# Performance work log

Hardware: AMD Instinct MI355X
Metric: run time of the kernel (lower is better)

## Reference

```python
import jax, jax.numpy as jnp
import numpy as np

HEADS = 8
HEAD_DIM = 64
INNER = HEADS * HEAD_DIM  # 512
DIM = 512
B, H, W = 8, 32, 32
KV_LEN, KV_DIM = 77, 1024


def group_norm(x, g, b, groups=32, eps=1e-6):
    # x: [B, C, H, W]
    Bx, C, Hx, Wx = x.shape
    xr = x.reshape(Bx, groups, C // groups, Hx, Wx)
    mu = xr.mean(axis=(2, 3, 4), keepdims=True)
    var = xr.var(axis=(2, 3, 4), keepdims=True)
    xr = (xr - mu) * jax.lax.rsqrt(var + eps)
    return xr.reshape(Bx, C, Hx, Wx) * g[None, :, None, None] + b[None, :, None, None]


def layer_norm(x, g, b, eps=1e-5):
    mu = x.mean(axis=-1, keepdims=True)
    var = x.var(axis=-1, keepdims=True)
    return (x - mu) * jax.lax.rsqrt(var + eps) * g + b


def attention(qx, kvx, Wq, Wk, Wv, Wo, bo):
    # qx: [B, Sq, dim_q], kvx: [B, Sk, dim_kv]
    q = qx @ Wq
    k = kvx @ Wk
    v = kvx @ Wv
    Bx, Sq, _ = q.shape
    Sk = k.shape[1]
    q = q.reshape(Bx, Sq, HEADS, HEAD_DIM)
    k = k.reshape(Bx, Sk, HEADS, HEAD_DIM)
    v = v.reshape(Bx, Sk, HEADS, HEAD_DIM)
    att = jnp.einsum('bqhd,bkhd->bhqk', q, k) * (HEAD_DIM ** -0.5)
    att = jax.nn.softmax(att.astype(jnp.float32), axis=-1).astype(q.dtype)
    o = jnp.einsum('bhqk,bkhd->bqhd', att, v).reshape(Bx, Sq, INNER)
    return o @ Wo + bo


def setup_inputs() -> dict:
    key = jax.random.key(0)
    ks = jax.random.split(key, 20)
    s = 0.02
    def n(k, shape):
        return jax.random.normal(k, shape, jnp.float32) * s
    return {
        'q': jax.random.normal(ks[0], (B, DIM, H, W), jnp.float32),
        'kv': jax.random.normal(ks[1], (B, KV_LEN, KV_DIM), jnp.float32),
        'gn_g': jnp.ones((DIM,), jnp.float32), 'gn_b': jnp.zeros((DIM,), jnp.float32),
        'ln2_g': jnp.ones((INNER,), jnp.float32), 'ln2_b': jnp.zeros((INNER,), jnp.float32),
        'ln3_g': jnp.ones((INNER,), jnp.float32), 'ln3_b': jnp.zeros((INNER,), jnp.float32),
        'ln4_g': jnp.ones((INNER,), jnp.float32), 'ln4_b': jnp.zeros((INNER,), jnp.float32),
        'fc_in_w': n(ks[2], (DIM, INNER)), 'fc_in_b': jnp.zeros((INNER,), jnp.float32),
        'fc_out_w': n(ks[3], (INNER, DIM)), 'fc_out_b': jnp.zeros((DIM,), jnp.float32),
        'a1_q': n(ks[4], (INNER, INNER)), 'a1_k': n(ks[5], (INNER, INNER)),
        'a1_v': n(ks[6], (INNER, INNER)), 'a1_o': n(ks[7], (INNER, INNER)),
        'a1_ob': jnp.zeros((INNER,), jnp.float32),
        'a2_q': n(ks[8], (INNER, INNER)), 'a2_k': n(ks[9], (KV_DIM, INNER)),
        'a2_v': n(ks[10], (KV_DIM, INNER)), 'a2_o': n(ks[11], (INNER, INNER)),
        'a2_ob': jnp.zeros((INNER,), jnp.float32),
        'ff_proj_w': n(ks[12], (INNER, INNER * 8)), 'ff_proj_b': jnp.zeros((INNER * 8,), jnp.float32),
        'ff_out_w': n(ks[13], (INNER * 4, INNER)), 'ff_out_b': jnp.zeros((INNER,), jnp.float32),
    }


def reference(q, kv, gn_g, gn_b, ln2_g, ln2_b, ln3_g, ln3_b, ln4_g, ln4_b,
              fc_in_w, fc_in_b, fc_out_w, fc_out_b,
              a1_q, a1_k, a1_v, a1_o, a1_ob,
              a2_q, a2_k, a2_v, a2_o, a2_ob,
              ff_proj_w, ff_proj_b, ff_out_w, ff_out_b):
    res = q
    Bx, C, Hx, Wx = q.shape
    x = group_norm(q, gn_g, gn_b)
    x = x.reshape(Bx, C, Hx * Wx).transpose(0, 2, 1)  # [B, S, C]
    x = x @ fc_in_w + fc_in_b
    t = layer_norm(x, ln2_g, ln2_b)
    x = attention(t, t, a1_q, a1_k, a1_v, a1_o, a1_ob) + x
    x = attention(layer_norm(x, ln3_g, ln3_b), kv, a2_q, a2_k, a2_v, a2_o, a2_ob) + x
    h = layer_norm(x, ln4_g, ln4_b) @ ff_proj_w + ff_proj_b
    a, gate = jnp.split(h, 2, axis=-1)
    x = (a * jax.nn.gelu(gate, approximate=False)) @ ff_out_w + ff_out_b + x
    x = x @ fc_out_w + fc_out_b
    x = x.transpose(0, 2, 1).reshape(Bx, C, Hx, Wx)
    return x + res
```

## Files before the change

### kernel.cpp

```cpp
#include <hip/hip_runtime.h>
#include <cstdint>
#include <cstddef>

typedef __attribute__((ext_vector_type(8))) short bf16x8;
typedef __attribute__((ext_vector_type(4))) short short4v;
typedef __attribute__((ext_vector_type(4))) float f32x4;

__device__ __forceinline__ short f2b(float f) {
    unsigned u = __builtin_bit_cast(unsigned, f);
    u = (u + 0x7FFFu + ((u >> 16) & 1u)) >> 16;
    return (short)u;
}
__device__ __forceinline__ float b2f(short s) {
    unsigned u = ((unsigned)(unsigned short)s) << 16;
    return __builtin_bit_cast(float, u);
}

__device__ __forceinline__ void gload16(const short* g, short* l) {
    __builtin_amdgcn_global_load_lds(
        (const __attribute__((address_space(1))) unsigned int*)g,
        (__attribute__((address_space(3))) unsigned int*)l, 16, 0, 0);
}

__device__ __forceinline__ float gelu_fast(float g) {
    float g2 = g * g;
    float gp = g * (0.7978845608f + 0.0356774081f * g2);
    float e = exp2f(2.885390082f * gp);
    float th = 1.f - 2.f / (e + 1.f);
    return 0.5f * g * (1.f + th);
}

__device__ __forceinline__ int pn_ffp(int n) {
    int m = (n < 2048) ? n : (n - 2048);
    int gofs = (n < 2048) ? 0 : 32;
    int x = m >> 6, c = m & 63;
    return x * 128 + ((c >> 5) << 6) + gofs + (c & 31);
}

struct PrepArgs {
    const float* src[12];
    short* dst[12];
    const float* kv;
    short* kvb;
    const float* fb;
    float* bp;
};

__global__ __launch_bounds__(256) void prep(PrepArgs a) {
    int t = blockIdx.x;
    int tid = threadIdx.x;
    if (t >= 6144) {
        if (t >= 6452) {
            int n = (t - 6452) * 256 + tid;
            if (n < 4096) a.bp[pn_ffp(n)] = a.fb[n];
            return;
        }
        int idx = (t - 6144) * 256 + tid;
        if (idx >= 78848) return;
        const float4* s = (const float4*)a.kv + (size_t)idx * 2;
        float4 va = s[0], vb = s[1];
        bf16x8 w;
        w[0] = f2b(va.x); w[1] = f2b(va.y); w[2] = f2b(va.z); w[3] = f2b(va.w);
        w[4] = f2b(vb.x); w[5] = f2b(vb.y); w[6] = f2b(vb.z); w[7] = f2b(vb.w);
        *(bf16x8*)(a.kvb + (size_t)idx * 8) = w;
        return;
    }
    const int jstart[12] = {0, 256, 512, 768, 1024, 1280, 1536, 1792, 2304, 2816, 3072, 5120};
    const int jK[12] = {512, 512, 512, 512, 512, 512, 512, 1024, 1024, 512, 512, 2048};
    const int jN[12] = {512, 512, 512, 512, 512, 512, 512, 512, 512, 512, 4096, 512};
    int j = 11;
#pragma unroll
    for (int i = 11; i >= 1; --i)
        if (t < jstart[i]) j = i - 1;
    int tx = t - jstart[j];
    int K = jK[j], N = jN[j];
    int tn = N >> 5;
    int n0 = (tx % tn) * 32, k0 = (tx / tn) * 32;
    const float* w = a.src[j];
    short* wt = a.dst[j];
    bool perm = (j == 10);

    __shared__ float tile[32][33];
    int cx = tid & 31, ty0 = tid >> 5;
#pragma unroll
    for (int i = 0; i < 4; ++i) {
        int r = ty0 + i * 8;
        tile[r][cx] = w[(size_t)(k0 + r) * N + n0 + cx];
    }
    __syncthreads();
    int r = tid >> 3;
    int kg = (tid & 7) * 4;
    int drow = perm ? pn_ffp(n0 + r) : (n0 + r);
    short4v o = {f2b(tile[kg][r]), f2b(tile[kg + 1][r]),
                 f2b(tile[kg + 2][r]), f2b(tile[kg + 3][r])};
    *(short4v*)&wt[(size_t)drow * K + k0 + kg] = o;
}

__global__ __launch_bounds__(256) void gn_stats(const float* __restrict__ q,
                                                const float* __restrict__ g,
                                                const float* __restrict__ bta,
                                                float* __restrict__ sc,
                                                float* __restrict__ sh) {
    int bb = blockIdx.x >> 5, gg = blockIdx.x & 31;
    const float4* src = (const float4*)(q + ((size_t)(bb * 512 + gg * 16)) * 1024);
    float s = 0.f, s2 = 0.f;
#pragma unroll
    for (int i = 0; i < 16; ++i) {
        float4 v = src[threadIdx.x + 256 * i];
        s += (v.x + v.y) + (v.z + v.w);
        s2 += (v.x * v.x + v.y * v.y) + (v.z * v.z + v.w * v.w);
    }
#pragma unroll
    for (int m = 1; m < 64; m <<= 1) {
        s += __shfl_xor(s, m);
        s2 += __shfl_xor(s2, m);
    }
    __shared__ float red[8];
    int wv = threadIdx.x >> 6;
    if ((threadIdx.x & 63) == 0) { red[wv] = s; red[4 + wv] = s2; }
    __syncthreads();
    if (threadIdx.x < 16) {
        float S = red[0] + red[1] + red[2] + red[3];
        float S2 = red[4] + red[5] + red[6] + red[7];
        float mu = S * (1.f / 16384.f);
        float var = S2 * (1.f / 16384.f) - mu * mu;
        float rs = rsqrtf(var + 1e-6f);
        int c = gg * 16 + threadIdx.x;
        float scale = rs * g[c];
        sc[bb * 512 + c] = scale;
        sh[bb * 512 + c] = bta[c] - mu * scale;
    }
}

__global__ __launch_bounds__(256) void gn_apply(const float* __restrict__ q,
                                                const float* __restrict__ sc,
                                                const float* __restrict__ sh,
                                                short* __restrict__ out) {
    __shared__ short tile[512][33];
    int b = blockIdx.x >> 5, st = blockIdx.x & 31;
    int s0 = st * 32;
    int sl = threadIdx.x & 31, cg = threadIdx.x >> 5;
    for (int c = cg; c < 512; c += 8) {
        float v = q[((size_t)(b * 512 + c)) * 1024 + s0 + sl];
        float y = v * sc[b * 512 + c] + sh[b * 512 + c];
        tile[c][sl] = f2b(y);
    }
    __syncthreads();
    int sr = threadIdx.x >> 3, ch = threadIdx.x & 7;
    short* orow = out + ((size_t)(b * 1024 + s0 + sr)) * 512;
    for (int c8 = ch * 64; c8 < ch * 64 + 64; c8 += 8) {
        bf16x8 o;
#pragma unroll
        for (int jj = 0; jj < 8; ++jj) o[jj] = tile[c8 + jj][sr];
        *(bf16x8*)&orow[c8] = o;
    }
}

__global__ __launch_bounds__(256) void ln_rows(const short* __restrict__ x,
                                               const float* __restrict__ g,
                                               const float* __restrict__ bta,
                                               short* __restrict__ out) {
    int row = blockIdx.x * 4 + (threadIdx.x >> 6);
    int lane = threadIdx.x & 63;
    bf16x8 v8 = *(const bf16x8*)(x + (size_t)row * 512 + lane * 8);
    float v[8];
#pragma unroll
    for (int j = 0; j < 8; ++j) v[j] = b2f(v8[j]);
    float s = 0.f, s2 = 0.f;
#pragma unroll
    for (int j = 0; j < 8; ++j) { s += v[j]; s2 += v[j] * v[j]; }
#pragma unroll
    for (int m = 1; m < 64; m <<= 1) {
        s += __shfl_xor(s, m);
        s2 += __shfl_xor(s2, m);
    }
    float mu = s * (1.f / 512.f);
    float var = s2 * (1.f / 512.f) - mu * mu;
    float rs = rsqrtf(var + 1e-5f);
    float4 ga = ((const float4*)g)[lane * 2], gb = ((const float4*)g)[lane * 2 + 1];
    float4 ba = ((const float4*)bta)[lane * 2], bb = ((const float4*)bta)[lane * 2 + 1];
    bf16x8 o;
    o[0] = f2b((v[0] - mu) * rs * ga.x + ba.x);
    o[1] = f2b((v[1] - mu) * rs * ga.y + ba.y);
    o[2] = f2b((v[2] - mu) * rs * ga.z + ba.z);
    o[3] = f2b((v[3] - mu) * rs * ga.w + ba.w);
    o[4] = f2b((v[4] - mu) * rs * gb.x + bb.x);
    o[5] = f2b((v[5] - mu) * rs * gb.y + bb.y);
    o[6] = f2b((v[6] - mu) * rs * gb.z + bb.z);
    o[7] = f2b((v[7] - mu) * rs * gb.w + bb.w);
    *(bf16x8*)(out + (size_t)row * 512 + lane * 8) = o;
}

template <int BN>
__global__ __launch_bounds__(256, 1) void gemm_gl(
    const short* __restrict__ A, const short* __restrict__ BT,
    int M, int N, int K,
    const float* __restrict__ bias,
    const short* __restrict__ addSrcB,
    short* __restrict__ outB,
    const float* __restrict__ resid,
    float* __restrict__ outFinal,
    int mode) {
    constexpr int FJ = BN / 32;
    constexpr int ASZ = 3 * 128 * 32;
    constexpr int BSZ = 3 * BN * 32;
    __shared__ __attribute__((aligned(16))) short smem[ASZ + BSZ];
    short* Asb = smem;
    short* Bsb = smem + ASZ;
    int tid = threadIdx.x;
    int wave = tid >> 6, lane = tid & 63;
    int wr = wave >> 1, wc = wave & 1;
    int m0 = blockIdx.y * 128, n0 = blockIdx.x * BN;
    f32x4 acc[4][FJ];
#pragma unroll
    for (int i = 0; i < 4; ++i)
#pragma unroll
        for (int j = 0; j < FJ; ++j) acc[i][j] = (f32x4){0.f, 0.f, 0.f, 0.f};

    int srow = tid >> 2;
    int scg = (((tid & 3) ^ ((tid >> 3) & 3)) << 3);
    int ar0 = m0 + srow; if (ar0 >= M) ar0 = M - 1;
    int ar1 = m0 + 64 + srow; if (ar1 >= M) ar1 = M - 1;
    const short* ag0 = A + (size_t)ar0 * K + scg;
    const short* ag1 = A + (size_t)ar1 * K + scg;
    const short* bg0 = BT + (size_t)(n0 + srow) * K + scg;
    const short* bg1 = BT + (size_t)(n0 + 64 + srow) * K + scg;
    int nk = K >> 5;

    auto stage = [&](int buf) {
        gload16(ag0, &Asb[buf * 4096 + wave * 512]);
        gload16(ag1, &Asb[buf * 4096 + 2048 + wave * 512]);
        gload16(bg0, &Bsb[buf * (BN * 32) + wave * 512]);
        if constexpr (BN == 128) gload16(bg1, &Bsb[buf * 4096 + 2048 + wave * 512]);
        ag0 += 32; ag1 += 32; bg0 += 32; bg1 += 32;
    };
    stage(0);
    stage(1);

    int lr = lane & 15, g = lane >> 4;

#define GL_STEP(KT, BUF)                                                          \
    {                                                                             \
        __builtin_amdgcn_sched_barrier(0);                                        \
        if ((KT) + 1 < nk) {                                                      \
            if constexpr (BN == 128)                                              \
                asm volatile("s_waitcnt vmcnt(4)" ::: "memory");                  \
            else                                                                  \
                asm volatile("s_waitcnt vmcnt(3)" ::: "memory");                  \
        } else {                                                                  \
            asm volatile("s_waitcnt vmcnt(0)" ::: "memory");                      \
        }                                                                         \
        __builtin_amdgcn_sched_barrier(0);                                        \
        __builtin_amdgcn_s_barrier();                                             \
        if ((KT) + 2 < nk) stage(((BUF) + 2) % 3);                                \
        bf16x8 af[4], bfr[FJ];                                                    \
        _Pragma("unroll") for (int i = 0; i < 4; ++i) {                           \
            int row = wr * 64 + i * 16 + lr;                                      \
            af[i] = *(const bf16x8*)&Asb[(BUF) * 4096 + row * 32 +                \
                                         ((g ^ ((row >> 1) & 3)) << 3)];          \
        }                                                                         \
        _Pragma("unroll") for (int j = 0; j < FJ; ++j) {                          \
            int row = wc * (BN / 2) + j * 16 + lr;                                \
            bfr[j] = *(const bf16x8*)&Bsb[(BUF) * (BN * 32) + row * 32 +          \
                                          ((g ^ ((row >> 1) & 3)) << 3)];         \
        }                                                                         \
        _Pragma("unroll") for (int i = 0; i < 4; ++i)                             \
            _Pragma("unroll") for (int j = 0; j < FJ; ++j)                        \
                acc[i][j] = __builtin_amdgcn_mfma_f32_16x16x32_bf16(              \
                    af[i], bfr[j], acc[i][j], 0, 0, 0);                           \
    }

    for (int kt = 0; kt < nk; kt += 3) {
        GL_STEP(kt, 0);
        if (kt + 1 < nk) GL_STEP(kt + 1, 1);
        if (kt + 2 < nk) GL_STEP(kt + 2, 2);
    }
#undef GL_STEP

    int lq = lane >> 4;
    if (mode == 1) {
#pragma unroll
        for (int i = 0; i < 4; ++i)
#pragma unroll
            for (int j = 0; j < FJ; ++j) {
                int mm0 = m0 + wr * 64 + i * 16 + lq * 4;
                int nn = n0 + wc * (BN / 2) + j * 16 + lr;
                int bb = mm0 >> 10, ss = mm0 & 1023;
                size_t oi = ((size_t)(bb * 512 + nn)) * 1024 + ss;
                float bv = bias ? bias[nn] : 0.f;
                float4 rv = *(const float4*)&resid[oi];
                float4 ov;
                ov.x = acc[i][j][0] + bv + rv.x;
                ov.y = acc[i][j][1] + bv + rv.y;
                ov.z = acc[i][j][2] + bv + rv.z;
                ov.w = acc[i][j][3] + bv + rv.w;
                *(float4*)&outFinal[oi] = ov;
            }
        return;
    }
    {
        constexpr int EC = BN + 4;
        float* ef = (float*)smem;
#pragma unroll
        for (int h = 0; h < 2; ++h) {
            __syncthreads();
            if (wr == h) {
#pragma unroll
                for (int i = 0; i < 4; ++i)
#pragma unroll
                    for (int j = 0; j < FJ; ++j)
#pragma unroll
                        for (int r = 0; r < 4; ++r)
                            ef[(i * 16 + lq * 4 + r) * EC + wc * (BN / 2) + j * 16 + lr] =
                                acc[i][j][r];
            }
            __syncthreads();
#pragma unroll
            for (int q = 0; q < BN / 16; ++q) {
                int idx = q * 256 + tid;
                int row = idx / (BN / 4);
                int cq = (idx % (BN / 4)) * 4;
                int mm = m0 + h * 64 + row;
                if (mm >= M) continue;
                int nn = n0 + cq;
                float4 v = *(float4*)&ef[row * EC + cq];
                if (bias) {
                    float4 b4 = *(const float4*)&bias[nn];
                    v.x += b4.x; v.y += b4.y; v.z += b4.z; v.w += b4.w;
                }
                size_t ig = (size_t)mm * N + nn;
                if (addSrcB) {
                    short4v a4 = *(const short4v*)&addSrcB[ig];
                    v.x += b2f(a4[0]); v.y += b2f(a4[1]);
                    v.z += b2f(a4[2]); v.w += b2f(a4[3]);
                }
                short4v o = {f2b(v.x), f2b(v.y), f2b(v.z), f2b(v.w)};
                *(short4v*)&outB[ig] = o;
            }
        }
    }
}

__global__ __launch_bounds__(512, 1) void gemm256w(
    const short* __restrict__ A, const short* __restrict__ BT,
    int M, int N, int K,
    const float* __restrict__ bias,
    short* __restrict__ outB,
    int mode) {
    __shared__ __attribute__((aligned(16))) short smem[3 * 4096 + 3 * 8192];
    short* Asb = smem;
    short* Bsb = smem + 12288;
    int tid = threadIdx.x;
    int wave = tid >> 6, lane = tid & 63;
    int wrM = wave >> 2, wcN = wave & 3;
    int m0 = blockIdx.y * 128, n0 = blockIdx.x * 256;
    f32x4 acc[4][4];
#pragma unroll
    for (int i = 0; i < 4; ++i)
#pragma unroll
        for (int j = 0; j < 4; ++j) acc[i][j] = (f32x4){0.f, 0.f, 0.f, 0.f};

    const short* gp[3];
    int ldsoff[3];
    bool isA[3];
#pragma unroll
    for (int s = 0; s < 3; ++s) {
        int qq = wave * 3 + s;
        bool a = qq < 8;
        int r = (a ? qq : qq - 8) * 16 + (lane >> 2);
        int sc = (((lane & 3) ^ ((r >> 1) & 3)) << 3);
        gp[s] = a ? (A + (size_t)(m0 + r) * K + sc)
                  : (BT + (size_t)(n0 + r) * K + sc);
        ldsoff[s] = (a ? qq : (qq - 8)) * 512;
        isA[s] = a;
    }
    int nk = K >> 5;
    auto stage = [&](int buf) {
#pragma unroll
        for (int s = 0; s < 3; ++s) {
            short* l = isA[s] ? &Asb[buf * 4096 + ldsoff[s]]
                              : &Bsb[buf * 8192 + ldsoff[s]];
            gload16(gp[s], l);
            gp[s] += 32;
        }
    };
    stage(0);
    stage(1);

    int lr = lane & 15, g = lane >> 4;

#define W8_STEP(KT, BUF)                                                          \
    {                                                                             \
        __builtin_amdgcn_sched_barrier(0);                                        \
        if ((KT) + 1 < nk) {                                                      \
            asm volatile("s_waitcnt vmcnt(3)" ::: "memory");                      \
        } else {                                                                  \
            asm volatile("s_waitcnt vmcnt(0)" ::: "memory");                      \
        }                                                                         \
        __builtin_amdgcn_sched_barrier(0);                                        \
        __builtin_amdgcn_s_barrier();                                             \
        if ((KT) + 2 < nk) stage(((BUF) + 2) % 3);                                \
        bf16x8 af[4], bfr[4];                                                     \
        _Pragma("unroll") for (int i = 0; i < 4; ++i) {                           \
            int row = wrM * 64 + i * 16 + lr;                                     \
            af[i] = *(const bf16x8*)&Asb[(BUF) * 4096 + row * 32 +                \
                                         ((g ^ ((row >> 1) & 3)) << 3)];          \
        }                                                                         \
        _Pragma("unroll") for (int j = 0; j < 4; ++j) {                           \
            int row = wcN * 64 + j * 16 + lr;                                     \
            bfr[j] = *(const bf16x8*)&Bsb[(BUF) * 8192 + row * 32 +               \
                                          ((g ^ ((row >> 1) & 3)) << 3)];         \
        }                                                                         \
        _Pragma("unroll") for (int i = 0; i < 4; ++i)                             \
            _Pragma("unroll") for (int j = 0; j < 4; ++j)                         \
                acc[i][j] = __builtin_amdgcn_mfma_f32_16x16x32_bf16(              \
                    af[i], bfr[j], acc[i][j], 0, 0, 0);                           \
    }

    for (int kt = 0; kt < nk; kt += 3) {
        W8_STEP(kt, 0);
        if (kt + 1 < nk) W8_STEP(kt + 1, 1);
        if (kt + 2 < nk) W8_STEP(kt + 2, 2);
    }
#undef W8_STEP

    int lq = lane >> 4;
    if (mode == 2) {
        short* eb = smem;
        int xhalf = wcN >> 1, half = wcN & 1;
        __syncthreads();
#pragma unroll
        for (int i = 0; i < 4; ++i)
#pragma unroll
            for (int j = 0; j < 2; ++j)
#pragma unroll
                for (int r = 0; r < 4; ++r) {
                    int slot = n0 + wcN * 64 + j * 16 + lr;
                    float a = acc[i][j][r] + bias[slot];
                    float gt = acc[i][j + 2][r] + bias[slot + 32];
                    float ge = gelu_fast(gt);
                    int row = wrM * 64 + i * 16 + lq * 4 + r;
                    int col = xhalf * 64 + half * 32 + j * 16 + lr;
                    eb[row * 136 + col] = f2b(a * ge);
                }
        __syncthreads();
#pragma unroll
        for (int q = 0; q < 4; ++q) {
            int idx = q * 512 + tid;
            int row = idx >> 4, cg = (idx & 15) * 8;
            bf16x8 o = *(bf16x8*)&eb[row * 136 + cg];
            *(bf16x8*)&outB[(size_t)(m0 + row) * 2048 + blockIdx.x * 128 + cg] = o;
        }
        return;
    }
    {
        float* ef = (float*)smem;
#pragma unroll
        for (int h = 0; h < 2; ++h) {
            __syncthreads();
            if (wrM == h) {
#pragma unroll
                for (int i = 0; i < 4; ++i)
#pragma unroll
                    for (int j = 0; j < 4; ++j)
#pragma unroll
                        for (int r = 0; r < 4; ++r)
                            ef[(i * 16 + lq * 4 + r) * 260 + wcN * 64 + j * 16 + lr] =
                                acc[i][j][r];
            }
            __syncthreads();
#pragma unroll
            for (int q = 0; q < 8; ++q) {
                int idx = q * 512 + tid;
                int row = idx >> 6;
                int cq = (idx & 63) * 4;
                float4 v = *(float4*)&ef[row * 260 + cq];
                int nn = n0 + cq;
                if (bias) {
                    float4 b4 = *(const float4*)&bias[nn];
                    v.x += b4.x; v.y += b4.y; v.z += b4.z; v.w += b4.w;
                }
                short4v o = {f2b(v.x), f2b(v.y), f2b(v.z), f2b(v.w)};
                *(short4v*)&outB[(size_t)(m0 + h * 64 + row) * N + nn] = o;
            }
        }
    }
}

__global__ __launch_bounds__(256, 1) void attn_mfma(const short* __restrict__ qp,
                                                    const short* __restrict__ kp,
                                                    const short* __restrict__ vp,
                                                    short* __restrict__ op,
                                                    int kv_len, int kvBatchRows,
                                                    int qStride, int kvStride) {
    __shared__ __attribute__((aligned(16))) short Kt[64][72];
    __shared__ __attribute__((aligned(16))) short Vt[64][72];
    __shared__ __attribute__((aligned(16))) short Pt[4][2][16][72];
    int tid = threadIdx.x, w = tid >> 6, lane = tid & 63;
    int g = lane >> 4, c = lane & 15;
    int bh = blockIdx.y, b = bh >> 3, h = bh & 7;
    int q0 = blockIdx.x * 128 + w * 16;

    const float QS = 0.125f * 1.44269504f;
    bf16x8 qa[2][2];
#pragma unroll
    for (int qi = 0; qi < 2; ++qi) {
        const short* qbase = qp + ((size_t)(b * 1024 + q0 + qi * 64 + c)) * qStride + h * 64;
        bf16x8 qr0 = *(const bf16x8*)(qbase + g * 8);
        bf16x8 qr1 = *(const bf16x8*)(qbase + 32 + g * 8);
#pragma unroll
        for (int j = 0; j < 8; ++j) {
            qa[qi][0][j] = f2b(b2f(qr0[j]) * QS);
            qa[qi][1][j] = f2b(b2f(qr1[j]) * QS);
        }
    }

    f32x4 oac[2][4];
#pragma unroll
    for (int qi = 0; qi < 2; ++qi)
#pragma unroll
        for (int dt = 0; dt < 4; ++dt) oac[qi][dt] = (f32x4){0.f, 0.f, 0.f, 0.f};
    float l[2][4];
#pragma unroll
    for (int qi = 0; qi < 2; ++qi)
#pragma unroll
        for (int r = 0; r < 4; ++r) l[qi][r] = 0.f;

    int skey = tid & 63, sd0 = (tid >> 6) * 16;
    int ntile = (kv_len + 63) >> 6;
    size_t kvbase = (size_t)b * kvBatchRows;

    bf16x8 k0, k1, v0, v1;
    {
        int krow = skey < kv_len ? skey : kv_len - 1;
        const short* kpp = kp + (kvbase + krow) * kvStride + h * 64 + sd0;
        const short* vpp = vp + (kvbase + krow) * kvStride + h * 64 + sd0;
        k0 = *(const bf16x8*)kpp; k1 = *(const bf16x8*)(kpp + 8);
        v0 = *(const bf16x8*)vpp; v1 = *(const bf16x8*)(vpp + 8);
    }

    for (int kt = 0; kt < ntile; ++kt) {
        __syncthreads();
        *(bf16x8*)&Kt[skey][sd0] = k0;
        *(bf16x8*)&Kt[skey][sd0 + 8] = k1;
#pragma unroll
        for (int j = 0; j < 8; ++j) {
            Vt[sd0 + j][skey] = v0[j];
            Vt[sd0 + 8 + j][skey] = v1[j];
        }
        __syncthreads();
        if (kt + 1 < ntile) {
            int krow = (kt + 1) * 64 + skey;
            if (krow >= kv_len) krow = kv_len - 1;
            const short* kpp = kp + (kvbase + krow) * kvStride + h * 64 + sd0;
            const short* vpp = vp + (kvbase + krow) * kvStride + h * 64 + sd0;
            k0 = *(const bf16x8*)kpp; k1 = *(const bf16x8*)(kpp + 8);
            v0 = *(const bf16x8*)vpp; v1 = *(const bf16x8*)(vpp + 8);
        }

        f32x4 s[2][4];
#pragma unroll
        for (int nt = 0; nt < 4; ++nt) {
            bf16x8 kb0 = *(const bf16x8*)&Kt[nt * 16 + c][g * 8];
            bf16x8 kb1 = *(const bf16x8*)&Kt[nt * 16 + c][32 + g * 8];
#pragma unroll
            for (int qi = 0; qi < 2; ++qi) {
                s[qi][nt] = __builtin_amdgcn_mfma_f32_16x16x32_bf16(
                    qa[qi][0], kb0, (f32x4){0.f, 0.f, 0.f, 0.f}, 0, 0, 0);
                s[qi][nt] = __builtin_amdgcn_mfma_f32_16x16x32_bf16(
                    qa[qi][1], kb1, s[qi][nt], 0, 0, 0);
            }
        }
        if (kt * 64 + 64 > kv_len) {
#pragma unroll
            for (int nt = 0; nt < 4; ++nt) {
                bool valid = kt * 64 + nt * 16 + c < kv_len;
#pragma unroll
                for (int qi = 0; qi < 2; ++qi)
#pragma unroll
                    for (int r = 0; r < 4; ++r) {
                        float pv = valid ? exp2f(s[qi][nt][r]) : 0.f;
                        s[qi][nt][r] = pv;
                        l[qi][r] += pv;
                    }
            }
        } else {
#pragma unroll
            for (int nt = 0; nt < 4; ++nt)
#pragma unroll
                for (int qi = 0; qi < 2; ++qi)
#pragma unroll
                    for (int r = 0; r < 4; ++r) {
                        float pv = exp2f(s[qi][nt][r]);
                        s[qi][nt][r] = pv;
                        l[qi][r] += pv;
                    }
        }

        bf16x8 pa[2][2];
#pragma unroll
        for (int qi = 0; qi < 2; ++qi) {
#pragma unroll
            for (int nt = 0; nt < 4; ++nt)
#pragma unroll
                for (int r = 0; r < 4; ++r)
                    Pt[w][qi][4 * g + r][nt * 16 + c] = f2b(s[qi][nt][r]);
        }
#pragma unroll
        for (int qi = 0; qi < 2; ++qi) {
            pa[qi][0] = *(const bf16x8*)&Pt[w][qi][c][g * 8];
            pa[qi][1] = *(const bf16x8*)&Pt[w][qi][c][32 + g * 8];
        }
#pragma unroll
        for (int dt = 0; dt < 4; ++dt) {
            bf16x8 vb0 = *(const bf16x8*)&Vt[dt * 16 + c][g * 8];
            bf16x8 vb1 = *(const bf16x8*)&Vt[dt * 16 + c][32 + g * 8];
#pragma unroll
            for (int qi = 0; qi < 2; ++qi) {
                oac[qi][dt] = __builtin_amdgcn_mfma_f32_16x16x32_bf16(pa[qi][0], vb0, oac[qi][dt], 0, 0, 0);
                oac[qi][dt] = __builtin_amdgcn_mfma_f32_16x16x32_bf16(pa[qi][1], vb1, oac[qi][dt], 0, 0, 0);
            }
        }
    }

#pragma unroll
    for (int mk = 1; mk < 16; mk <<= 1)
#pragma unroll
        for (int qi = 0; qi < 2; ++qi)
#pragma unroll
            for (int r = 0; r < 4; ++r) l[qi][r] += __shfl_xor(l[qi][r], mk);
#pragma unroll
    for (int qi = 0; qi < 2; ++qi)
#pragma unroll
        for (int r = 0; r < 4; ++r) {
            float inv = 1.f / l[qi][r];
            short* orow = op + ((size_t)(b * 1024 + q0 + qi * 64 + 4 * g + r)) * 512 + h * 64;
#pragma unroll
            for (int dt = 0; dt < 4; ++dt)
                orow[dt * 16 + c] = f2b(oac[qi][dt][r] * inv);
        }
}

extern "C" void kernel_launch(void* const* d_in, const int* in_sizes, int n_in,
                              void* d_out, int out_size, void* d_ws, size_t ws_size,
                              hipStream_t stream) {
    (void)in_sizes; (void)n_in; (void)out_size; (void)ws_size;
    const float* q_in = (const float*)d_in[0];
    const float* kv_in = (const float*)d_in[1];
    const float* gn_g = (const float*)d_in[2];
    const float* gn_b = (const float*)d_in[3];
    const float* ln2_g = (const float*)d_in[4];
    const float* ln2_b = (const float*)d_in[5];
    const float* ln3_g = (const float*)d_in[6];
    const float* ln3_b = (const float*)d_in[7];
    const float* ln4_g = (const float*)d_in[8];
    const float* ln4_b = (const float*)d_in[9];
    const float* fc_in_w = (const float*)d_in[10];
    const float* fc_in_b = (const float*)d_in[11];
    const float* fc_out_w = (const float*)d_in[12];
    const float* fc_out_b = (const float*)d_in[13];
    const float* a1_qw = (const float*)d_in[14];
    const float* a1_kw = (const float*)d_in[15];
    const float* a1_vw = (const float*)d_in[16];
    const float* a1_ow = (const float*)d_in[17];
    const float* a1_ob = (const float*)d_in[18];
    const float* a2_qw = (const float*)d_in[19];
    const float* a2_kw = (const float*)d_in[20];
    const float* a2_vw = (const float*)d_in[21];
    const float* a2_ow = (const float*)d_in[22];
    const float* a2_ob = (const float*)d_in[23];
    const float* ffp_w = (const float*)d_in[24];
    const float* ffp_b = (const float*)d_in[25];
    const float* ffo_w = (const float*)d_in[26];
    const float* ffo_b = (const float*)d_in[27];
    float* out = (float*)d_out;

    char* p = (char*)d_ws;
    auto alloc = [&](size_t n) {
        char* r = p;
        p += (n + 255) & ~(size_t)255;
        return r;
    };
    short* wt_fci = (short*)alloc((size_t)512 * 512 * 2);
    short* wt_fco = (short*)alloc((size_t)512 * 512 * 2);
    short* wt_qkv = (short*)alloc((size_t)1536 * 512 * 2);
    short* wt_a1o = (short*)alloc((size_t)512 * 512 * 2);
    short* wt_a2q = (short*)alloc((size_t)512 * 512 * 2);
    short* wt_kv2 = (short*)alloc((size_t)1024 * 1024 * 2);
    short* wt_a2o = (short*)alloc((size_t)512 * 512 * 2);
    short* wt_ffp = (short*)alloc((size_t)4096 * 512 * 2);
    short* wt_ffo = (short*)alloc((size_t)512 * 2048 * 2);
    float* biasP = (float*)alloc((size_t)4096 * 4);
    short* xb = (short*)alloc((size_t)8192 * 512 * 2);
    short* tb = (short*)alloc((size_t)8192 * 512 * 2);
    short* qkvbuf = (short*)alloc((size_t)8192 * 1536 * 2);
    short* qbuf = (short*)alloc((size_t)8192 * 512 * 2);
    short* kvpbuf = (short*)alloc((size_t)616 * 1024 * 2);
    short* obuf = (short*)alloc((size_t)8192 * 512 * 2);
    short* kvb = (short*)alloc((size_t)616 * 1024 * 2);
    short* ggb = (short*)alloc((size_t)8192 * 2048 * 2);
    float* gnsc = (float*)alloc((size_t)8 * 512 * 4);
    float* gnsh = (float*)alloc((size_t)8 * 512 * 4);

    PrepArgs pa;
    pa.src[0] = fc_in_w;  pa.dst[0] = wt_fci;
    pa.src[1] = fc_out_w; pa.dst[1] = wt_fco;
    pa.src[2] = a1_qw;    pa.dst[2] = wt_qkv;
    pa.src[3] = a1_kw;    pa.dst[3] = wt_qkv + (size_t)512 * 512;
    pa.src[4] = a1_vw;    pa.dst[4] = wt_qkv + (size_t)1024 * 512;
    pa.src[5] = a1_ow;    pa.dst[5] = wt_a1o;
    pa.src[6] = a2_qw;    pa.dst[6] = wt_a2q;
    pa.src[7] = a2_kw;    pa.dst[7] = wt_kv2;
    pa.src[8] = a2_vw;    pa.dst[8] = wt_kv2 + (size_t)512 * 1024;
    pa.src[9] = a2_ow;    pa.dst[9] = wt_a2o;
    pa.src[10] = ffp_w;   pa.dst[10] = wt_ffp;
    pa.src[11] = ffo_w;   pa.dst[11] = wt_ffo;
    pa.kv = kv_in; pa.kvb = kvb; pa.fb = ffp_b; pa.bp = biasP;
    prep<<<6468, 256, 0, stream>>>(pa);

    auto gemm128n = [&](const short* A, const short* BT, int M, int N, int K,
                        const float* bias, const short* addSrcB, short* outB,
                        const float* resid, float* outFinal, int mode) {
        dim3 g(N / 128, (M + 127) / 128);
        gemm_gl<128><<<g, 256, 0, stream>>>(A, BT, M, N, K, bias, addSrcB, outB,
                                            resid, outFinal, mode);
    };
    auto gemm64n = [&](const short* A, const short* BT, int M, int N, int K,
                       const float* bias, const short* addSrcB, short* outB,
                       const float* resid, float* outFinal, int mode) {
        dim3 g(N / 64, (M + 127) / 128);
        gemm_gl<64><<<g, 256, 0, stream>>>(A, BT, M, N, K, bias, addSrcB, outB,
                                           resid, outFinal, mode);
    };

    gn_stats<<<256, 256, 0, stream>>>(q_in, gn_g, gn_b, gnsc, gnsh);
    gn_apply<<<256, 256, 0, stream>>>(q_in, gnsc, gnsh, tb);
    gemm64n(tb, wt_fci, 8192, 512, 512, fc_in_b, nullptr, xb, nullptr, nullptr, 0);
    ln_rows<<<2048, 256, 0, stream>>>(xb, ln2_g, ln2_b, tb);
    gemm256w<<<dim3(6, 64), 512, 0, stream>>>(tb, wt_qkv, 8192, 1536, 512,
                                              nullptr, qkvbuf, 0);
    attn_mfma<<<dim3(8, 64), 256, 0, stream>>>(qkvbuf, qkvbuf + 512, qkvbuf + 1024, obuf,
                                               1024, 1024, 1536, 1536);
    gemm64n(obuf, wt_a1o, 8192, 512, 512, a1_ob, xb, xb, nullptr, nullptr, 0);
    ln_rows<<<2048, 256, 0, stream>>>(xb, ln3_g, ln3_b, tb);
    gemm64n(tb, wt_a2q, 8192, 512, 512, nullptr, nullptr, qbuf, nullptr, nullptr, 0);
    gemm128n(kvb, wt_kv2, 616, 1024, 1024, nullptr, nullptr, kvpbuf, nullptr, nullptr, 0);
    attn_mfma<<<dim3(8, 64), 256, 0, stream>>>(qbuf, kvpbuf, kvpbuf + 512, obuf,
                                               77, 77, 512, 1024);
    gemm64n(obuf, wt_a2o, 8192, 512, 512, a2_ob, xb, xb, nullptr, nullptr, 0);
    ln_rows<<<2048, 256, 0, stream>>>(xb, ln4_g, ln4_b, tb);
    gemm256w<<<dim3(16, 64), 512, 0, stream>>>(tb, wt_ffp, 8192, 4096, 512,
                                               biasP, ggb, 2);
    gemm128n(ggb, wt_ffo, 8192, 512, 2048, ffo_b, xb, tb, nullptr, nullptr, 0);
    gemm64n(tb, wt_fco, 8192, 512, 512, fc_out_b, nullptr, nullptr, q_in, out, 1);
}
```

Baseline: 298.2 us.

## Widen attention KV tiles to 128 and retile projection GEMMs

The attention kernel now stages 128 keys per shared-memory tile and processes them in two 64-key halves, halving the number of sync/load rounds per query block. The 512-wide GEMMs switch from 64-column tiles to 128-column tiles. The FF-out GEMM moves to the 256-wide kernel, which gains a residual-add input for this purpose. Larger tiles cut launch count and redundant A reloads, but they also mean fewer blocks (only 128 for FF-out) and more LDS use, which can lower occupancy and parallelism.

Measured after the change: 307.7 us. 3.2% more time.

```diff
diff --git a/kernel.cpp b/kernel.cpp
--- a/kernel.cpp
+++ b/kernel.cpp
@@ -345,6 +345,7 @@
     const short* __restrict__ A, const short* __restrict__ BT,
     int M, int N, int K,
     const float* __restrict__ bias,
+    const short* __restrict__ addSrcB,
     short* __restrict__ outB,
     int mode) {
     __shared__ __attribute__((aligned(16))) short smem[3 * 4096 + 3 * 8192];
@@ -480,8 +481,14 @@
                     float4 b4 = *(const float4*)&bias[nn];
                     v.x += b4.x; v.y += b4.y; v.z += b4.z; v.w += b4.w;
                 }
+                size_t ig = (size_t)(m0 + h * 64 + row) * N + nn;
+                if (addSrcB) {
+                    short4v a4 = *(const short4v*)&addSrcB[ig];
+                    v.x += b2f(a4[0]); v.y += b2f(a4[1]);
+                    v.z += b2f(a4[2]); v.w += b2f(a4[3]);
+                }
                 short4v o = {f2b(v.x), f2b(v.y), f2b(v.z), f2b(v.w)};
-                *(short4v*)&outB[(size_t)(m0 + h * 64 + row) * N + nn] = o;
+                *(short4v*)&outB[ig] = o;
             }
         }
     }
@@ -493,8 +500,8 @@
                                                     short* __restrict__ op,
                                                     int kv_len, int kvBatchRows,
                                                     int qStride, int kvStride) {
-    __shared__ __attribute__((aligned(16))) short Kt[64][72];
-    __shared__ __attribute__((aligned(16))) short Vt[64][72];
+    __shared__ __attribute__((aligned(16))) short Kt[128][72];
+    __shared__ __attribute__((aligned(16))) short Vt[64][136];
     __shared__ __attribute__((aligned(16))) short Pt[4][2][16][72];
     int tid = threadIdx.x, w = tid >> 6, lane = tid & 63;
     int g = lane >> 4, c = lane & 15;
@@ -527,98 +534,112 @@
         for (int r = 0; r < 4; ++r) l[qi][r] = 0.f;
 
     int skey = tid & 63, sd0 = (tid >> 6) * 16;
-    int ntile = (kv_len + 63) >> 6;
+    int ntile = (kv_len + 127) >> 7;
     size_t kvbase = (size_t)b * kvBatchRows;
 
-    bf16x8 k0, k1, v0, v1;
-    {
-        int krow = skey < kv_len ? skey : kv_len - 1;
+    bf16x8 k0[2], k1[2], v0[2], v1[2];
+#pragma unroll
+    for (int t2 = 0; t2 < 2; ++t2) {
+        int krow = skey + t2 * 64;
+        if (krow >= kv_len) krow = kv_len - 1;
         const short* kpp = kp + (kvbase + krow) * kvStride + h * 64 + sd0;
         const short* vpp = vp + (kvbase + krow) * kvStride + h * 64 + sd0;
-        k0 = *(const bf16x8*)kpp; k1 = *(const bf16x8*)(kpp + 8);
-        v0 = *(const bf16x8*)vpp; v1 = *(const bf16x8*)(vpp + 8);
+        k0[t2] = *(const bf16x8*)kpp; k1[t2] = *(const bf16x8*)(kpp + 8);
+        v0[t2] = *(const bf16x8*)vpp; v1[t2] = *(const bf16x8*)(vpp + 8);
     }
 
     for (int kt = 0; kt < ntile; ++kt) {
         __syncthreads();
-        *(bf16x8*)&Kt[skey][sd0] = k0;
-        *(bf16x8*)&Kt[skey][sd0 + 8] = k1;
-#pragma unroll
-        for (int j = 0; j < 8; ++j) {
-            Vt[sd0 + j][skey] = v0[j];
-            Vt[sd0 + 8 + j][skey] = v1[j];
+#pragma unroll
+        for (int t2 = 0; t2 < 2; ++t2) {
+            int key = t2 * 64 + skey;
+            *(bf16x8*)&Kt[key][sd0] = k0[t2];
+            *(bf16x8*)&Kt[key][sd0 + 8] = k1[t2];
+#pragma unroll
+            for (int j = 0; j < 8; ++j) {
+                Vt[sd0 + j][key] = v0[t2][j];
+                Vt[sd0 + 8 + j][key] = v1[t2][j];
+            }
         }
         __syncthreads();
         if (kt + 1 < ntile) {
-            int krow = (kt + 1) * 64 + skey;
-            if (krow >= kv_len) krow = kv_len - 1;
-            const short* kpp = kp + (kvbase + krow) * kvStride + h * 64 + sd0;
-            const short* vpp = vp + (kvbase + krow) * kvStride + h * 64 + sd0;
-            k0 = *(const bf16x8*)kpp; k1 = *(const bf16x8*)(kpp + 8);
-            v0 = *(const bf16x8*)vpp; v1 = *(const bf16x8*)(vpp + 8);
-        }
-
-        f32x4 s[2][4];
-#pragma unroll
-        for (int nt = 0; nt < 4; ++nt) {
-            bf16x8 kb0 = *(const bf16x8*)&Kt[nt * 16 + c][g * 8];
-            bf16x8 kb1 = *(const bf16x8*)&Kt[nt * 16 + c][32 + g * 8];
+#pragma unroll
+            for (int t2 = 0; t2 < 2; ++t2) {
+                int krow = (kt + 1) * 128 + t2 * 64 + skey;
+                if (krow >= kv_len) krow = kv_len - 1;
+                const short* kpp = kp + (kvbase + krow) * kvStride + h * 64 + sd0;
+                const short* vpp = vp + (kvbase + krow) * kvStride + h * 64 + sd0;
+                k0[t2] = *(const bf16x8*)kpp; k1[t2] = *(const bf16x8*)(kpp + 8);
+                v0[t2] = *(const bf16x8*)vpp; v1[t2] = *(const bf16x8*)(vpp + 8);
+            }
+        }
+
+#pragma unroll
+        for (int half = 0; half < 2; ++half) {
+            f32x4 s[2][4];
+#pragma unroll
+            for (int nt = 0; nt < 4; ++nt) {
+                int row = half * 64 + nt * 16 + c;
+                bf16x8 kb0 = *(const bf16x8*)&Kt[row][g * 8];
+                bf16x8 kb1 = *(const bf16x8*)&Kt[row][32 + g * 8];
+#pragma unroll
+                for (int qi = 0; qi < 2; ++qi) {
+                    s[qi][nt] = __builtin_amdgcn_mfma_f32_16x16x32_bf16(
+                        qa[qi][0], kb0, (f32x4){0.f, 0.f, 0.f, 0.f}, 0, 0, 0);
+                    s[qi][nt] = __builtin_amdgcn_mfma_f32_16x16x32_bf16(
+                        qa[qi][1], kb1, s[qi][nt], 0, 0, 0);
+                }
+            }
+            if (kt * 128 + half * 64 + 64 > kv_len) {
+#pragma unroll
+                for (int nt = 0; nt < 4; ++nt) {
+                    bool valid = kt * 128 + half * 64 + nt * 16 + c < kv_len;
+#pragma unroll
+                    for (int qi = 0; qi < 2; ++qi)
+#pragma unroll
+                        for (int r = 0; r < 4; ++r) {
+                            float pv = valid ? exp2f(s[qi][nt][r]) : 0.f;
+                            s[qi][nt][r] = pv;
+                            l[qi][r] += pv;
+                        }
+                }
+            } else {
+#pragma unroll
+                for (int nt = 0; nt < 4; ++nt)
+#pragma unroll
+                    for (int qi = 0; qi < 2; ++qi)
+#pragma unroll
+                        for (int r = 0; r < 4; ++r) {
+                            float pv = exp2f(s[qi][nt][r]);
+                            s[qi][nt][r] = pv;
+                            l[qi][r] += pv;
+                        }
+            }
+
+            bf16x8 pa[2][2];
 #pragma unroll
             for (int qi = 0; qi < 2; ++qi) {
-                s[qi][nt] = __builtin_amdgcn_mfma_f32_16x16x32_bf16(
-                    qa[qi][0], kb0, (f32x4){0.f, 0.f, 0.f, 0.f}, 0, 0, 0);
-                s[qi][nt] = __builtin_amdgcn_mfma_f32_16x16x32_bf16(
-                    qa[qi][1], kb1, s[qi][nt], 0, 0, 0);
-            }
-        }
-        if (kt * 64 + 64 > kv_len) {
-#pragma unroll
-            for (int nt = 0; nt < 4; ++nt) {
-                bool valid = kt * 64 + nt * 16 + c < kv_len;
-#pragma unroll
-                for (int qi = 0; qi < 2; ++qi)
-#pragma unroll
-                    for (int r = 0; r < 4; ++r) {
-                        float pv = valid ? exp2f(s[qi][nt][r]) : 0.f;
-                        s[qi][nt][r] = pv;
-                        l[qi][r] += pv;
-                    }
-            }
-        } else {
-#pragma unroll
-            for (int nt = 0; nt < 4; ++nt)
-#pragma unroll
-                for (int qi = 0; qi < 2; ++qi)
-#pragma unroll
-                    for (int r = 0; r < 4; ++r) {
-                        float pv = exp2f(s[qi][nt][r]);
-                        s[qi][nt][r] = pv;
-                        l[qi][r] += pv;
-                    }
-        }
-
-        bf16x8 pa[2][2];
-#pragma unroll
-        for (int qi = 0; qi < 2; ++qi) {
-#pragma unroll
-            for (int nt = 0; nt < 4; ++nt)
-#pragma unroll
-                for (int r = 0; r < 4; ++r)
-                    Pt[w][qi][4 * g + r][nt * 16 + c] = f2b(s[qi][nt][r]);
-        }
-#pragma unroll
-        for (int qi = 0; qi < 2; ++qi) {
-            pa[qi][0] = *(const bf16x8*)&Pt[w][qi][c][g * 8];
-            pa[qi][1] = *(const bf16x8*)&Pt[w][qi][c][32 + g * 8];
-        }
-#pragma unroll
-        for (int dt = 0; dt < 4; ++dt) {
-            bf16x8 vb0 = *(const bf16x8*)&Vt[dt * 16 + c][g * 8];
-            bf16x8 vb1 = *(const bf16x8*)&Vt[dt * 16 + c][32 + g * 8];
+#pragma unroll
+                for (int nt = 0; nt < 4; ++nt)
+#pragma unroll
+                    for (int r = 0; r < 4; ++r)
+                        Pt[w][qi][4 * g + r][nt * 16 + c] = f2b(s[qi][nt][r]);
+            }
 #pragma unroll
             for (int qi = 0; qi < 2; ++qi) {
-                oac[qi][dt] = __builtin_amdgcn_mfma_f32_16x16x32_bf16(pa[qi][0], vb0, oac[qi][dt], 0, 0, 0);
-                oac[qi][dt] = __builtin_amdgcn_mfma_f32_16x16x32_bf16(pa[qi][1], vb1, oac[qi][dt], 0, 0, 0);
+                pa[qi][0] = *(const bf16x8*)&Pt[w][qi][c][g * 8];
+                pa[qi][1] = *(const bf16x8*)&Pt[w][qi][c][32 + g * 8];
+            }
+#pragma unroll
+            for (int dt = 0; dt < 4; ++dt) {
+                int drow = dt * 16 + c;
+                bf16x8 vb0 = *(const bf16x8*)&Vt[drow][half * 64 + g * 8];
+                bf16x8 vb1 = *(const bf16x8*)&Vt[drow][half * 64 + 32 + g * 8];
+#pragma unroll
+                for (int qi = 0; qi < 2; ++qi) {
+                    oac[qi][dt] = __builtin_amdgcn_mfma_f32_16x16x32_bf16(pa[qi][0], vb0, oac[qi][dt], 0, 0, 0);
+                    oac[qi][dt] = __builtin_amdgcn_mfma_f32_16x16x32_bf16(pa[qi][1], vb1, oac[qi][dt], 0, 0, 0);
+                }
             }
         }
     }
@@ -725,32 +746,26 @@
         gemm_gl<128><<<g, 256, 0, stream>>>(A, BT, M, N, K, bias, addSrcB, outB,
                                             resid, outFinal, mode);
     };
-    auto gemm64n = [&](const short* A, const short* BT, int M, int N, int K,
-                       const float* bias, const short* addSrcB, short* outB,
-                       const float* resid, float* outFinal, int mode) {
-        dim3 g(N / 64, (M + 127) / 128);
-        gemm_gl<64><<<g, 256, 0, stream>>>(A, BT, M, N, K, bias, addSrcB, outB,
-                                           resid, outFinal, mode);
-    };
 
     gn_stats<<<256, 256, 0, stream>>>(q_in, gn_g, gn_b, gnsc, gnsh);
     gn_apply<<<256, 256, 0, stream>>>(q_in, gnsc, gnsh, tb);
-    gemm64n(tb, wt_fci, 8192, 512, 512, fc_in_b, nullptr, xb, nullptr, nullptr, 0);
+    gemm128n(tb, wt_fci, 8192, 512, 512, fc_in_b, nullptr, xb, nullptr, nullptr, 0);
     ln_rows<<<2048, 256, 0, stream>>>(xb, ln2_g, ln2_b, tb);
     gemm256w<<<dim3(6, 64), 512, 0, stream>>>(tb, wt_qkv, 8192, 1536, 512,
-                                              nullptr, qkvbuf, 0);
+                                              nullptr, nullptr, qkvbuf, 0);
     attn_mfma<<<dim3(8, 64), 256, 0, stream>>>(qkvbuf, qkvbuf + 512, qkvbuf + 1024, obuf,
                                                1024, 1024, 1536, 1536);
-    gemm64n(obuf, wt_a1o, 8192, 512, 512, a1_ob, xb, xb, nullptr, nullptr, 0);
+    gemm128n(obuf, wt_a1o, 8192, 512, 512, a1_ob, xb, xb, nullptr, nullptr, 0);
     ln_rows<<<2048, 256, 0, stream>>>(xb, ln3_g, ln3_b, tb);
-    gemm64n(tb, wt_a2q, 8192, 512, 512, nullptr, nullptr, qbuf, nullptr, nullptr, 0);
+    gemm128n(tb, wt_a2q, 8192, 512, 512, nullptr, nullptr, qbuf, nullptr, nullptr, 0);
     gemm128n(kvb, wt_kv2, 616, 1024, 1024, nullptr, nullptr, kvpbuf, nullptr, nullptr, 0);
     attn_mfma<<<dim3(8, 64), 256, 0, stream>>>(qbuf, kvpbuf, kvpbuf + 512, obuf,
                                                77, 77, 512, 1024);
-    gemm64n(obuf, wt_a2o, 8192, 512, 512, a2_ob, xb, xb, nullptr, nullptr, 0);
+    gemm128n(obuf, wt_a2o, 8192, 512, 512, a2_ob, xb, xb, nullptr, nullptr, 0);
     ln_rows<<<2048, 256, 0, stream>>>(xb, ln4_g, ln4_b, tb);
     gemm256w<<<dim3(16, 64), 512, 0, stream>>>(tb, wt_ffp, 8192, 4096, 512,
-                                               biasP, ggb, 2);
-    gemm128n(ggb, wt_ffo, 8192, 512, 2048, ffo_b, xb, tb, nullptr, nullptr, 0);
-    gemm64n(tb, wt_fco, 8192, 512, 512, fc_out_b, nullptr, nullptr, q_in, out, 1);
-}
+                                               biasP, nullptr, ggb, 2);
+    gemm256w<<<dim3(2, 64), 512, 0, stream>>>(ggb, wt_ffo, 8192, 512, 2048,
+                                              ffo_b, xb, tb, 0);
+    gemm128n(tb, wt_fco, 8192, 512, 512, fc_out_b, nullptr, nullptr, q_in, out, 1);
+}
```
